# Kernel optimization log

Measured on AMD Instinct MI355X. Metric: run time of the kernel, lower is better.

The kernel has to match this reference:

```python
import jax, jax.numpy as jnp
import numpy as np

NHEADS = 16

def setup_inputs() -> dict:
    key = jax.random.key(0)
    ks = jax.random.split(key, 11)
    B, S, D = 2, 2048, 1024
    std = 1.0 / np.sqrt(D)
    return {
        "query": jax.random.normal(ks[0], (B, S, D), jnp.float32),
        "key":   jax.random.normal(ks[1], (B, S, D), jnp.float32),
        "value": jax.random.normal(ks[2], (B, S, D), jnp.float32),
        "Wq": jax.random.normal(ks[3], (D, D), jnp.float32) * std,
        "bq": jax.random.normal(ks[4], (D,), jnp.float32) * std,
        "Wk": jax.random.normal(ks[5], (D, D), jnp.float32) * std,
        "bk": jax.random.normal(ks[6], (D,), jnp.float32) * std,
        "Wv": jax.random.normal(ks[7], (D, D), jnp.float32) * std,
        "bv": jax.random.normal(ks[8], (D,), jnp.float32) * std,
        "Wo": jax.random.normal(ks[9], (D, D), jnp.float32) * std,
        "bo": jax.random.normal(ks[10], (D,), jnp.float32) * std,
    }

def reference(query, key, value, Wq, bq, Wk, bk, Wv, bv, Wo, bo):
    B, Sq, D = query.shape
    Sk = key.shape[1]
    H = NHEADS
    hd = D // H
    q = (query @ Wq + bq).reshape(B, Sq, H, hd)
    k = (key @ Wk + bk).reshape(B, Sk, H, hd)
    v = (value @ Wv + bv).reshape(B, Sk, H, hd)
    # Explicit [B,H,Sq,Sk] score tensor, as in the original
    score = jnp.einsum('bqhd,bkhd->bhqk', q, k)
    # masked=True: causal mask applied before scaling (equivalent: -inf/c = -inf)
    cmask = jnp.triu(jnp.ones((Sq, Sk), dtype=bool), k=1)
    score = jnp.where(cmask, -jnp.inf, score)
    # NOTE: original divides by sqrt(score.shape[-1]) == sqrt(Sk), NOT sqrt(head_dim)
    scale = jnp.float32(1.0 / np.sqrt(Sk))
    att = jax.nn.softmax(score * scale, axis=-1)
    ret = jnp.einsum('bhqk,bkhd->bqhd', att, v).reshape(B, Sq, D)
    return ret @ Wo + bo
```

## Files before the change

### kernel.cpp

```cpp
#include <hip/hip_runtime.h>
#include <stdint.h>

typedef unsigned short u16;
typedef unsigned int u32;
typedef u32 u32x4 __attribute__((ext_vector_type(4)));
typedef __bf16 bf16x8 __attribute__((ext_vector_type(8)));
typedef __bf16 bf16x4 __attribute__((ext_vector_type(4)));
typedef float f32x4 __attribute__((ext_vector_type(4)));

__device__ __forceinline__ u16 f2bf(float f) {
  u32 u = __float_as_uint(f);
  u = (u + 0x7fffu + ((u >> 16) & 1u)) >> 16;
  return (u16)u;
}

__device__ __forceinline__ void gload16(const void* g, void* l) {
  __builtin_amdgcn_global_load_lds(
      (const __attribute__((address_space(1))) void*)g,
      (__attribute__((address_space(3))) void*)l, 16, 0, 0);
}

__global__ __launch_bounds__(256) void prep_k(
    const float* __restrict__ q, const float* __restrict__ k,
    const float* __restrict__ v, u16* __restrict__ dst,
    const float* __restrict__ w0, const float* __restrict__ w1,
    const float* __restrict__ w2, const float* __restrict__ w3,
    u16* __restrict__ wt) {
  const int id = blockIdx.x;
  if (id < 6144) {
    const int y = id >> 11;
    const int x = id & 2047;
    const float* s = (y == 0) ? q : (y == 1) ? k : v;
    u16* d = dst + (size_t)y * 4194304u;
    int e = (x * 256 + threadIdx.x) * 8;
    float4 a = *(const float4*)(s + e);
    float4 b = *(const float4*)(s + e + 4);
    uint4 o;
    o.x = (u32)f2bf(a.x) | ((u32)f2bf(a.y) << 16);
    o.y = (u32)f2bf(a.z) | ((u32)f2bf(a.w) << 16);
    o.z = (u32)f2bf(b.x) | ((u32)f2bf(b.y) << 16);
    o.w = (u32)f2bf(b.z) | ((u32)f2bf(b.w) << 16);
    *(uint4*)(d + e) = o;
    return;
  }
  __shared__ float tile[64][65];
  const int t = id - 6144;
  const int z = t >> 8;
  const int rem = t & 255;
  const int x0 = (rem & 15) * 64, y0 = (rem >> 4) * 64;
  const float* W = (z == 0) ? w0 : (z == 1) ? w1 : (z == 2) ? w2 : w3;
  u16* Wt = wt + (size_t)z * 1048576u;
  const int tx = threadIdx.x & 63, ty = threadIdx.x >> 6;
#pragma unroll
  for (int j = 0; j < 16; ++j)
    tile[ty + j * 4][tx] = W[(size_t)(y0 + ty + j * 4) * 1024 + x0 + tx];
  __syncthreads();
#pragma unroll
  for (int j = 0; j < 16; ++j)
    Wt[(size_t)(x0 + ty + j * 4) * 1024 + y0 + tx] = f2bf(tile[tx][ty + j * 4]);
}

__global__ __launch_bounds__(256, 3) void gemm_proj(
    const u16* __restrict__ Xb, const u16* __restrict__ Wt,
    const float* __restrict__ bqp, const float* __restrict__ bkp,
    const float* __restrict__ bvp,
    u16* __restrict__ Qb, u16* __restrict__ Kb, u16* __restrict__ VtG,
    float qsc) {
  const int z = blockIdx.z;
  const u16 *A, *Bt;
  const float* bias;
  u16* C;
  int N, bm, bn;
  float osc = 1.f;
  bool rowb = false;
  if (z < 2) {
    A = Xb + (size_t)z * 4194304u;
    Bt = Wt + (size_t)z * 1048576u;
    bias = z ? bkp : bqp;
    C = z ? Kb : Qb;
    N = 1024;
    bm = blockIdx.x * 128;
    bn = blockIdx.y * 128;
    if (z == 0) osc = qsc;
  } else {
    A = Wt + 2u * 1048576u;
    Bt = Xb + 2u * 4194304u;
    bias = bvp;
    C = VtG;
    N = 4096;
    bm = blockIdx.y * 128;
    bn = blockIdx.x * 128;
    rowb = true;
  }

  __shared__ __align__(16) u16 ldsA[128 * 64];
  __shared__ __align__(16) u16 ldsB[128 * 64];

  const int tid = threadIdx.x;
  const int lane = tid & 63, wv = tid >> 6;
  const int wr = wv >> 1, wc = wv & 1;
  const int l15 = lane & 15, l4 = lane >> 4;

  const f32x4 zero4 = {0.f, 0.f, 0.f, 0.f};
  f32x4 acc[4][4];
#pragma unroll
  for (int i = 0; i < 4; ++i)
#pragma unroll
    for (int j = 0; j < 4; ++j) acc[i][j] = zero4;

  for (int kt = 0; kt < 16; ++kt) {
    __syncthreads();
#pragma unroll
    for (int g = 0; g < 4; ++g) {
      int p = g * 256 + tid;
      int row = p >> 3;
      int ss = (p & 7) ^ (row & 7);
      gload16(A + (size_t)(bm + row) * 1024 + kt * 64 + ss * 8,
              (char*)ldsA + (g * 256 + wv * 64) * 16);
    }
#pragma unroll
    for (int g = 0; g < 4; ++g) {
      int p = g * 256 + tid;
      int row = p >> 3;
      int ss = (p & 7) ^ (row & 7);
      gload16(Bt + (size_t)(bn + row) * 1024 + kt * 64 + ss * 8,
              (char*)ldsB + (g * 256 + wv * 64) * 16);
    }
    __syncthreads();

    bf16x8 af[4][2], bfr[4][2];
#pragma unroll
    for (int mf = 0; mf < 4; ++mf) {
      int row = wr * 64 + mf * 16 + l15;
#pragma unroll
      for (int ks = 0; ks < 2; ++ks) {
        int byt = row * 128 + ((ks * 64 + l4 * 16) ^ ((row & 7) << 4));
        af[mf][ks] = *(const bf16x8*)((const char*)ldsA + byt);
      }
    }
#pragma unroll
    for (int nf = 0; nf < 4; ++nf) {
      int row = wc * 64 + nf * 16 + l15;
#pragma unroll
      for (int ks = 0; ks < 2; ++ks) {
        int byt = row * 128 + ((ks * 64 + l4 * 16) ^ ((row & 7) << 4));
        bfr[nf][ks] = *(const bf16x8*)((const char*)ldsB + byt);
      }
    }
#pragma unroll
    for (int mf = 0; mf < 4; ++mf)
#pragma unroll
      for (int nf = 0; nf < 4; ++nf) {
        acc[mf][nf] = __builtin_amdgcn_mfma_f32_16x16x32_bf16(
            af[mf][0], bfr[nf][0], acc[mf][nf], 0, 0, 0);
        acc[mf][nf] = __builtin_amdgcn_mfma_f32_16x16x32_bf16(
            af[mf][1], bfr[nf][1], acc[mf][nf], 0, 0, 0);
      }
  }

  float bcol[4];
  if (!rowb) {
#pragma unroll
    for (int nf = 0; nf < 4; ++nf)
      bcol[nf] = bias[bn + wc * 64 + nf * 16 + l15];
  }
#pragma unroll
  for (int mf = 0; mf < 4; ++mf) {
#pragma unroll
    for (int i = 0; i < 4; ++i) {
      int r = bm + wr * 64 + mf * 16 + l4 * 4 + i;
      float br = rowb ? bias[r] : 0.f;
#pragma unroll
      for (int nf = 0; nf < 4; ++nf) {
        int c = bn + wc * 64 + nf * 16 + l15;
        float val = (acc[mf][nf][i] + (rowb ? br : bcol[nf])) * osc;
        C[(size_t)r * N + c] = f2bf(val);
      }
    }
  }
}

__global__ __launch_bounds__(256, 3) void gemm_out(
    const u16* __restrict__ A, const u16* __restrict__ Bt,
    const float* __restrict__ bias, float* __restrict__ C) {
  __shared__ __align__(16) u16 ldsA[128 * 64];
  __shared__ __align__(16) u16 ldsB[128 * 64];

  const int tid = threadIdx.x;
  const int lane = tid & 63, wv = tid >> 6;
  const int wr = wv >> 1, wc = wv & 1;
  const int l15 = lane & 15, l4 = lane >> 4;
  const int bm = blockIdx.x * 128, bn = blockIdx.y * 128;

  const f32x4 zero4 = {0.f, 0.f, 0.f, 0.f};
  f32x4 acc[4][4];
#pragma unroll
  for (int i = 0; i < 4; ++i)
#pragma unroll
    for (int j = 0; j < 4; ++j) acc[i][j] = zero4;

  for (int kt = 0; kt < 16; ++kt) {
    __syncthreads();
#pragma unroll
    for (int g = 0; g < 4; ++g) {
      int p = g * 256 + tid;
      int row = p >> 3;
      int ss = (p & 7) ^ (row & 7);
      gload16(A + (size_t)(bm + row) * 1024 + kt * 64 + ss * 8,
              (char*)ldsA + (g * 256 + wv * 64) * 16);
    }
#pragma unroll
    for (int g = 0; g < 4; ++g) {
      int p = g * 256 + tid;
      int row = p >> 3;
      int ss = (p & 7) ^ (row & 7);
      gload16(Bt + (size_t)(bn + row) * 1024 + kt * 64 + ss * 8,
              (char*)ldsB + (g * 256 + wv * 64) * 16);
    }
    __syncthreads();

    bf16x8 af[4][2], bfr[4][2];
#pragma unroll
    for (int mf = 0; mf < 4; ++mf) {
      int row = wr * 64 + mf * 16 + l15;
#pragma unroll
      for (int ks = 0; ks < 2; ++ks) {
        int byt = row * 128 + ((ks * 64 + l4 * 16) ^ ((row & 7) << 4));
        af[mf][ks] = *(const bf16x8*)((const char*)ldsA + byt);
      }
    }
#pragma unroll
    for (int nf = 0; nf < 4; ++nf) {
      int row = wc * 64 + nf * 16 + l15;
#pragma unroll
      for (int ks = 0; ks < 2; ++ks) {
        int byt = row * 128 + ((ks * 64 + l4 * 16) ^ ((row & 7) << 4));
        bfr[nf][ks] = *(const bf16x8*)((const char*)ldsB + byt);
      }
    }
#pragma unroll
    for (int mf = 0; mf < 4; ++mf)
#pragma unroll
      for (int nf = 0; nf < 4; ++nf) {
        acc[mf][nf] = __builtin_amdgcn_mfma_f32_16x16x32_bf16(
            af[mf][0], bfr[nf][0], acc[mf][nf], 0, 0, 0);
        acc[mf][nf] = __builtin_amdgcn_mfma_f32_16x16x32_bf16(
            af[mf][1], bfr[nf][1], acc[mf][nf], 0, 0, 0);
      }
  }

  float bcol[4];
#pragma unroll
  for (int nf = 0; nf < 4; ++nf)
    bcol[nf] = bias[bn + wc * 64 + nf * 16 + l15];
#pragma unroll
  for (int mf = 0; mf < 4; ++mf) {
#pragma unroll
    for (int i = 0; i < 4; ++i) {
      int r = bm + wr * 64 + mf * 16 + l4 * 4 + i;
#pragma unroll
      for (int nf = 0; nf < 4; ++nf) {
        int c = bn + wc * 64 + nf * 16 + l15;
        C[(size_t)r * 1024 + c] = acc[mf][nf][i] + bcol[nf];
      }
    }
  }
}

__global__ __launch_bounds__(256, 4) void attn_k(
    const u16* __restrict__ Q, const u16* __restrict__ Kb,
    const u16* __restrict__ Vt, u16* __restrict__ ctx) {
  const int id = blockIdx.x + (blockIdx.y << 5);
  const int xcd = id & 7;
  const int kk = id >> 3;
  const int bh = xcd * 4 + (kk & 3);
  const int qt = 31 - (kk >> 2);
  const int b = bh >> 4, h = bh & 15;
  const int tid = threadIdx.x;
  const int lane = tid & 63, wv = tid >> 6;
  const int l15 = lane & 15, l4 = lane >> 4;

  __shared__ __align__(16) u16 Kt[2][64 * 64];
  __shared__ __align__(16) u16 Vl[2][64 * 64];

  const u16* KB = Kb + (size_t)(b * 2048) * 1024 + h * 64;
  const u16* VB = Vt + (size_t)(h * 64) * 4096 + b * 2048;

  const u16* qp =
      Q + (size_t)(b * 2048 + qt * 64 + wv * 16 + l15) * 1024 + h * 64;
  bf16x8 qf0 = *(const bf16x8*)(qp + l4 * 8);
  bf16x8 qf1 = *(const bf16x8*)(qp + 32 + l4 * 8);

  const f32x4 zero4 = {0.f, 0.f, 0.f, 0.f};
  f32x4 oacc[4];
#pragma unroll
  for (int i = 0; i < 4; ++i) oacc[i] = zero4;
  f32x4 lacc = zero4;

  const u32x4 onesw = {0x3F803F80u, 0x3F803F80u, 0x3F803F80u, 0x3F803F80u};
  const bf16x8 onesf = __builtin_bit_cast(bf16x8, onesw);

  auto issueKV = [&](int jt, int bufi) {
    const u16* kb = KB + (size_t)(jt * 64) * 1024;
#pragma unroll
    for (int g = 0; g < 2; ++g) {
      int p = g * 256 + tid;
      int row = p >> 3;
      int key = (row & 3) | (((row >> 3) & 1) << 2);
      int ss = (p & 7) ^ key;
      gload16(kb + (size_t)row * 1024 + ss * 8,
              (char*)(&Kt[bufi][0]) + (g * 256 + wv * 64) * 16);
    }
#pragma unroll
    for (int g = 0; g < 2; ++g) {
      int p = g * 256 + tid;
      int d = p >> 3;
      int ss = (p & 7) ^ (d & 7);
      gload16(VB + (size_t)d * 4096 + jt * 64 + ss * 8,
              (char*)(&Vl[bufi][0]) + (g * 256 + wv * 64) * 16);
    }
  };

  issueKV(0, 0);
  for (int j = 0; j <= qt; ++j) {
    const int cur = j & 1;
    __syncthreads();
    if (j < qt) issueKV(j + 1, cur ^ 1);

    f32x4 p4[4];
    __builtin_amdgcn_s_setprio(1);
#pragma unroll
    for (int nt = 0; nt < 4; ++nt) {
      int row = ((nt & 2) << 4) + ((nt & 1) << 2) + 8 * (l15 >> 2) + (l15 & 3);
      int key = (row & 3) | (((row >> 3) & 1) << 2);
      int sw = key << 4;
      const char* kr = (const char*)&Kt[cur][0] + row * 128;
      bf16x8 k0 = *(const bf16x8*)(kr + ((l4 * 16) ^ sw));
      bf16x8 k1 = *(const bf16x8*)(kr + ((64 + l4 * 16) ^ sw));
      f32x4 s = zero4;
      s = __builtin_amdgcn_mfma_f32_16x16x32_bf16(k0, qf0, s, 0, 0, 0);
      s = __builtin_amdgcn_mfma_f32_16x16x32_bf16(k1, qf1, s, 0, 0, 0);
      p4[nt] = s;
    }
    __builtin_amdgcn_s_setprio(0);

    if (j == qt) {
#pragma unroll
      for (int nt = 0; nt < 4; ++nt) {
        int kvb = ((nt & 2) << 4) + ((nt & 1) << 2) + 8 * l4;
#pragma unroll
        for (int i = 0; i < 4; ++i)
          if (kvb + i > wv * 16 + l15) p4[nt][i] = -1e30f;
      }
    }

#pragma unroll
    for (int nt = 0; nt < 4; ++nt)
#pragma unroll
      for (int i = 0; i < 4; ++i) p4[nt][i] = exp2f(p4[nt][i]);

    bf16x4 c0 = __builtin_convertvector(p4[0], bf16x4);
    bf16x4 c1 = __builtin_convertvector(p4[1], bf16x4);
    bf16x4 c2 = __builtin_convertvector(p4[2], bf16x4);
    bf16x4 c3 = __builtin_convertvector(p4[3], bf16x4);
    bf16x8 pa0 = __builtin_shufflevector(c0, c1, 0, 1, 2, 3, 4, 5, 6, 7);
    bf16x8 pa1 = __builtin_shufflevector(c2, c3, 0, 1, 2, 3, 4, 5, 6, 7);

    __builtin_amdgcn_s_setprio(1);
    lacc = __builtin_amdgcn_mfma_f32_16x16x32_bf16(pa0, onesf, lacc, 0, 0, 0);
    lacc = __builtin_amdgcn_mfma_f32_16x16x32_bf16(pa1, onesf, lacc, 0, 0, 0);
#pragma unroll
    for (int nt = 0; nt < 4; ++nt) {
      int d = nt * 16 + l15;
      int sw = (d & 7) << 4;
      const char* vr = (const char*)&Vl[cur][0] + d * 128;
      bf16x8 v0 = *(const bf16x8*)(vr + ((l4 * 16) ^ sw));
      bf16x8 v1 = *(const bf16x8*)(vr + ((64 + l4 * 16) ^ sw));
      oacc[nt] = __builtin_amdgcn_mfma_f32_16x16x32_bf16(pa0, v0, oacc[nt], 0, 0, 0);
      oacc[nt] = __builtin_amdgcn_mfma_f32_16x16x32_bf16(pa1, v1, oacc[nt], 0, 0, 0);
    }
    __builtin_amdgcn_s_setprio(0);
  }

  u16* cb = ctx + (size_t)(b * 2048 + qt * 64 + wv * 16) * 1024 + h * 64;
#pragma unroll
  for (int i = 0; i < 4; ++i) {
    float iv = 1.f / lacc[i];
    int r = l4 * 4 + i;
#pragma unroll
    for (int nt = 0; nt < 4; ++nt)
      cb[(size_t)r * 1024 + nt * 16 + l15] = f2bf(oacc[nt][i] * iv);
  }
}

extern "C" void kernel_launch(void* const* d_in, const int* in_sizes, int n_in,
                              void* d_out, int out_size, void* d_ws,
                              size_t ws_size, hipStream_t stream) {
  const float* q  = (const float*)d_in[0];
  const float* k  = (const float*)d_in[1];
  const float* v  = (const float*)d_in[2];
  const float* Wq = (const float*)d_in[3];
  const float* bq = (const float*)d_in[4];
  const float* Wk = (const float*)d_in[5];
  const float* bk = (const float*)d_in[6];
  const float* Wv = (const float*)d_in[7];
  const float* bv = (const float*)d_in[8];
  const float* Wo = (const float*)d_in[9];
  const float* bo = (const float*)d_in[10];

  char* ws = (char*)d_ws;
  u16* Xb  = (u16*)ws;
  u16* Wt  = (u16*)(ws + 25165824);
  u16* VtG = (u16*)(ws + 33554432);
  u16* ctx = Xb;
  u16* Qb  = (u16*)d_out;
  u16* Kb  = Qb + 4194304;

  const float SC2A = 0.0318793585f;

  prep_k<<<dim3(7168), 256, 0, stream>>>(q, k, v, Xb, Wq, Wk, Wv, Wo, Wt);
  gemm_proj<<<dim3(32, 8, 3), 256, 0, stream>>>(Xb, Wt, bq, bk, bv, Qb, Kb,
                                                VtG, SC2A);
  attn_k<<<dim3(32, 32), 256, 0, stream>>>(Qb, Kb, VtG, ctx);
  gemm_out<<<dim3(32, 8), 256, 0, stream>>>(ctx, Wt + 3 * 1048576, bo,
                                            (float*)d_out);
}
```

Measured before the change: 104.9 us.

## Fuse fp32-to-bf16 activation conversion into projection GEMM loads

The projection GEMM now loads fp32 query/key/value directly into LDS via global_load_lds and converts to bf16 when reading fragments, so the separate activation-conversion pass in prep_k is removed. This drops one full write and read of the bf16 activation buffers. In exchange the GEMM reads twice as many bytes per activation tile, LDS use grows to 48KB, and conversion work moves into the inner loop. It also raises wave priority around the MFMA block.

```diff
diff --git a/kernel.cpp b/kernel.cpp
--- a/kernel.cpp
+++ b/kernel.cpp
@@ -21,30 +21,11 @@
 }
 
 __global__ __launch_bounds__(256) void prep_k(
-    const float* __restrict__ q, const float* __restrict__ k,
-    const float* __restrict__ v, u16* __restrict__ dst,
     const float* __restrict__ w0, const float* __restrict__ w1,
     const float* __restrict__ w2, const float* __restrict__ w3,
     u16* __restrict__ wt) {
-  const int id = blockIdx.x;
-  if (id < 6144) {
-    const int y = id >> 11;
-    const int x = id & 2047;
-    const float* s = (y == 0) ? q : (y == 1) ? k : v;
-    u16* d = dst + (size_t)y * 4194304u;
-    int e = (x * 256 + threadIdx.x) * 8;
-    float4 a = *(const float4*)(s + e);
-    float4 b = *(const float4*)(s + e + 4);
-    uint4 o;
-    o.x = (u32)f2bf(a.x) | ((u32)f2bf(a.y) << 16);
-    o.y = (u32)f2bf(a.z) | ((u32)f2bf(a.w) << 16);
-    o.z = (u32)f2bf(b.x) | ((u32)f2bf(b.y) << 16);
-    o.w = (u32)f2bf(b.z) | ((u32)f2bf(b.w) << 16);
-    *(uint4*)(d + e) = o;
-    return;
-  }
   __shared__ float tile[64][65];
-  const int t = id - 6144;
+  const int t = blockIdx.x;
   const int z = t >> 8;
   const int rem = t & 255;
   const int x0 = (rem & 15) * 64, y0 = (rem >> 4) * 64;
@@ -61,21 +42,23 @@
 }
 
 __global__ __launch_bounds__(256, 3) void gemm_proj(
-    const u16* __restrict__ Xb, const u16* __restrict__ Wt,
+    const float* __restrict__ qin, const float* __restrict__ kin,
+    const float* __restrict__ vin, const u16* __restrict__ Wt,
     const float* __restrict__ bqp, const float* __restrict__ bkp,
     const float* __restrict__ bvp,
     u16* __restrict__ Qb, u16* __restrict__ Kb, u16* __restrict__ VtG,
     float qsc) {
   const int z = blockIdx.z;
-  const u16 *A, *Bt;
+  const float* Xf;
+  const u16* Wb;
   const float* bias;
   u16* C;
   int N, bm, bn;
   float osc = 1.f;
   bool rowb = false;
   if (z < 2) {
-    A = Xb + (size_t)z * 4194304u;
-    Bt = Wt + (size_t)z * 1048576u;
+    Xf = z ? kin : qin;
+    Wb = Wt + (size_t)z * 1048576u;
     bias = z ? bkp : bqp;
     C = z ? Kb : Qb;
     N = 1024;
@@ -83,8 +66,8 @@
     bn = blockIdx.y * 128;
     if (z == 0) osc = qsc;
   } else {
-    A = Wt + 2u * 1048576u;
-    Bt = Xb + 2u * 4194304u;
+    Wb = Wt + 2u * 1048576u;
+    Xf = vin;
     bias = bvp;
     C = VtG;
     N = 4096;
@@ -93,8 +76,9 @@
     rowb = true;
   }
 
-  __shared__ __align__(16) u16 ldsA[128 * 64];
-  __shared__ __align__(16) u16 ldsB[128 * 64];
+  __shared__ __align__(16) char lds[49152];
+  char* ldsF = lds;
+  char* ldsH = lds + 32768;
 
   const int tid = threadIdx.x;
   const int lane = tid & 63, wv = tid >> 6;
@@ -110,21 +94,26 @@
 
   for (int kt = 0; kt < 16; ++kt) {
     __syncthreads();
-#pragma unroll
-    for (int g = 0; g < 4; ++g) {
-      int p = g * 256 + tid;
-      int row = p >> 3;
-      int ss = (p & 7) ^ (row & 7);
-      gload16(A + (size_t)(bm + row) * 1024 + kt * 64 + ss * 8,
-              (char*)ldsA + (g * 256 + wv * 64) * 16);
-    }
-#pragma unroll
-    for (int g = 0; g < 4; ++g) {
-      int p = g * 256 + tid;
-      int row = p >> 3;
-      int ss = (p & 7) ^ (row & 7);
-      gload16(Bt + (size_t)(bn + row) * 1024 + kt * 64 + ss * 8,
-              (char*)ldsB + (g * 256 + wv * 64) * 16);
+    {
+      const int fbase = (z < 2) ? bm : bn;
+#pragma unroll
+      for (int g = 0; g < 8; ++g) {
+        int p = g * 256 + tid;
+        int row = p >> 4;
+        int c = p & 15;
+        int ss = c ^ ((row & 7) << 1);
+        gload16(Xf + (size_t)(fbase + row) * 1024 + kt * 64 + ss * 4,
+                ldsF + (g * 256 + wv * 64) * 16);
+      }
+      const int hbase = (z < 2) ? bn : bm;
+#pragma unroll
+      for (int g = 0; g < 4; ++g) {
+        int p = g * 256 + tid;
+        int row = p >> 3;
+        int ss = (p & 7) ^ (row & 7);
+        gload16(Wb + (size_t)(hbase + row) * 1024 + kt * 64 + ss * 8,
+                ldsH + (g * 256 + wv * 64) * 16);
+      }
     }
     __syncthreads();
 
@@ -134,8 +123,19 @@
       int row = wr * 64 + mf * 16 + l15;
 #pragma unroll
       for (int ks = 0; ks < 2; ++ks) {
-        int byt = row * 128 + ((ks * 64 + l4 * 16) ^ ((row & 7) << 4));
-        af[mf][ks] = *(const bf16x8*)((const char*)ldsA + byt);
+        if (z < 2) {
+          int sw = (row & 7) << 5;
+          const char* rp = ldsF + row * 256;
+          int off = (ks * 128 + l4 * 32) ^ sw;
+          f32x4 a = *(const f32x4*)(rp + off);
+          f32x4 b = *(const f32x4*)(rp + off + 16);
+          bf16x4 ca = __builtin_convertvector(a, bf16x4);
+          bf16x4 cb = __builtin_convertvector(b, bf16x4);
+          af[mf][ks] = __builtin_shufflevector(ca, cb, 0, 1, 2, 3, 4, 5, 6, 7);
+        } else {
+          int byt = row * 128 + ((ks * 64 + l4 * 16) ^ ((row & 7) << 4));
+          af[mf][ks] = *(const bf16x8*)(ldsH + byt);
+        }
       }
     }
 #pragma unroll
@@ -143,10 +143,22 @@
       int row = wc * 64 + nf * 16 + l15;
 #pragma unroll
       for (int ks = 0; ks < 2; ++ks) {
-        int byt = row * 128 + ((ks * 64 + l4 * 16) ^ ((row & 7) << 4));
-        bfr[nf][ks] = *(const bf16x8*)((const char*)ldsB + byt);
-      }
-    }
+        if (z < 2) {
+          int byt = row * 128 + ((ks * 64 + l4 * 16) ^ ((row & 7) << 4));
+          bfr[nf][ks] = *(const bf16x8*)(ldsH + byt);
+        } else {
+          int sw = (row & 7) << 5;
+          const char* rp = ldsF + row * 256;
+          int off = (ks * 128 + l4 * 32) ^ sw;
+          f32x4 a = *(const f32x4*)(rp + off);
+          f32x4 b = *(const f32x4*)(rp + off + 16);
+          bf16x4 ca = __builtin_convertvector(a, bf16x4);
+          bf16x4 cb = __builtin_convertvector(b, bf16x4);
+          bfr[nf][ks] = __builtin_shufflevector(ca, cb, 0, 1, 2, 3, 4, 5, 6, 7);
+        }
+      }
+    }
+    __builtin_amdgcn_s_setprio(1);
 #pragma unroll
     for (int mf = 0; mf < 4; ++mf)
 #pragma unroll
@@ -156,6 +168,7 @@
         acc[mf][nf] = __builtin_amdgcn_mfma_f32_16x16x32_bf16(
             af[mf][1], bfr[nf][1], acc[mf][nf], 0, 0, 0);
       }
+    __builtin_amdgcn_s_setprio(0);
   }
 
   float bcol[4];
@@ -409,18 +422,17 @@
   const float* bo = (const float*)d_in[10];
 
   char* ws = (char*)d_ws;
-  u16* Xb  = (u16*)ws;
+  u16* ctx = (u16*)ws;
   u16* Wt  = (u16*)(ws + 25165824);
   u16* VtG = (u16*)(ws + 33554432);
-  u16* ctx = Xb;
   u16* Qb  = (u16*)d_out;
   u16* Kb  = Qb + 4194304;
 
   const float SC2A = 0.0318793585f;
 
-  prep_k<<<dim3(7168), 256, 0, stream>>>(q, k, v, Xb, Wq, Wk, Wv, Wo, Wt);
-  gemm_proj<<<dim3(32, 8, 3), 256, 0, stream>>>(Xb, Wt, bq, bk, bv, Qb, Kb,
-                                                VtG, SC2A);
+  prep_k<<<dim3(1024), 256, 0, stream>>>(Wq, Wk, Wv, Wo, Wt);
+  gemm_proj<<<dim3(32, 8, 3), 256, 0, stream>>>(q, k, v, Wt, bq, bk, bv,
+                                                Qb, Kb, VtG, SC2A);
   attn_k<<<dim3(32, 32), 256, 0, stream>>>(Qb, Kb, VtG, ctx);
   gemm_out<<<dim3(32, 8), 256, 0, stream>>>(ctx, Wt + 3 * 1048576, bo,
                                             (float*)d_out);
```

Result: slower. 135.1 us (+28.8%).
